# Kernel optimization log

Hardware: AMD Instinct MI355X
Metric: run time of the kernel (lower is better)

## Reference

```python
import jax, jax.numpy as jnp
import numpy as np

NUM, K = 5, 3
IN_DIM, D_OUT = 512, 512
N_U, BATCH, GATED_IN = 64, 8192, 576
NB = NUM + K + 1  # 9 basis channels (num+k splines + 1 SiLU base)
TERM_SIZES = (4, 8)
TERM_MULTS = (32768, 16384)  # 4*32768 + 8*16384 = 262144 = D_OUT*IN_DIM
WDIM = 128


def extend_grid(grid, k):
    # grid: (S, num+1) -> (S, num+1+2k), appending k knots each side with uniform spacing h
    h = (grid[:, -1:] - grid[:, :1]) / (grid.shape[1] - 1)
    left = grid[:, :1] + h * jnp.arange(-k, 0, dtype=grid.dtype)
    right = grid[:, -1:] + h * jnp.arange(1, k + 1, dtype=grid.dtype)
    return jnp.concatenate([left, grid, right], axis=1)


def B_batch(x, grid, k):
    # Cox-de-Boor recursion. x: (S, B), grid: (S, G) extended. Returns (S, G-k-1, B).
    xg = x[:, None, :]
    g = grid[:, :, None]
    v = ((xg >= g[:, :-1]) & (xg < g[:, 1:])).astype(x.dtype)
    for p in range(1, k + 1):
        v = (xg - g[:, :-(p + 1)]) / (g[:, p:-1] - g[:, :-(p + 1)]) * v[:, :-1] \
          + (g[:, p + 1:] - xg) / (g[:, p + 1:] - g[:, 1:-p]) * v[:, 1:]
    return v


def lazy_P(terms, mults, perm, w):
    # emlp-style lazy equivariant projector: permute rows, apply small block
    # projectors with multiplicities, un-permute. w: (R, C).
    invperm = jnp.argsort(perm)
    wp = w[perm]
    outs, off = [], 0
    for P, m in zip(terms, mults):
        s = P.shape[0]
        blk = wp[off:off + m * s].reshape(m, s, -1)
        outs.append(jnp.einsum('ij,mjc->mic', P, blk).reshape(m * s, -1))
        off += m * s
    return jnp.concatenate(outs, axis=0)[invperm]


def setup_inputs() -> dict:
    key = jax.random.key(0)
    ks = jax.random.split(key, 12)
    x = jax.random.normal(ks[0], (BATCH, GATED_IN), dtype=jnp.float32)
    grid = jnp.tile(jnp.linspace(-1.0, 1.0, NUM + 1, dtype=jnp.float32)[None, :], (N_U, 1))
    linear_weight = 0.05 * jax.random.normal(ks[1], (D_OUT, NB * IN_DIM), dtype=jnp.float32)
    linear_bias = 0.05 * jax.random.normal(ks[2], (D_OUT,), dtype=jnp.float32)
    P_term_a = 0.3 * jax.random.normal(ks[3], (TERM_SIZES[0], TERM_SIZES[0]), dtype=jnp.float32)
    P_term_b = 0.3 * jax.random.normal(ks[4], (TERM_SIZES[1], TERM_SIZES[1]), dtype=jnp.float32)
    Pb = (1.0 / np.sqrt(D_OUT)) * jax.random.normal(ks[5], (D_OUT, D_OUT), dtype=jnp.float32)
    bi_basis = 0.01 * jax.random.normal(ks[6], (WDIM, D_OUT, D_OUT), dtype=jnp.float32)
    bi_w = jax.random.normal(ks[7], (WDIM,), dtype=jnp.float32)
    u = jnp.sort(jax.random.randint(ks[8], (N_U,), 0, GATED_IN))
    indices = jax.random.randint(ks[9], (IN_DIM,), 0, N_U)
    perm = jax.random.permutation(ks[10], D_OUT * IN_DIM)
    return {"x": x, "grid": grid, "linear_weight": linear_weight, "linear_bias": linear_bias,
            "P_term_a": P_term_a, "P_term_b": P_term_b, "Pb": Pb,
            "bi_basis": bi_basis, "bi_w": bi_w, "u": u, "indices": indices, "perm": perm}


def reference(x, grid, linear_weight, linear_bias, P_term_a, P_term_b, Pb, bi_basis, bi_w, u, indices, perm):
    batch = x.shape[0]
    # gather gate scalars and build spline + base activations
    gs = x[:, u].T                                   # (S, B)
    eg = extend_grid(grid, K)                        # (S, num+1+2k)
    sp = B_batch(gs, eg, K)                          # (S, num+k, B)
    sp = jnp.transpose(sp, (2, 1, 0))                # (B, num+k, S)
    sb = jax.nn.silu(gs).T[:, None, :]               # (B, 1, S)
    g = jnp.concatenate([sp, sb], axis=1)            # (B, NB, S)
    g = g[:, :, indices]                             # (B, NB, in_dim) gather via inverse indices
    acts = (g * x[:, None, :IN_DIM]).reshape(batch, -1)  # (B, NB*in_dim)
    # equivariant weight projection
    w_r = linear_weight.reshape(D_OUT, NB, IN_DIM).transpose(0, 2, 1).reshape(D_OUT * IN_DIM, NB)
    W_r = lazy_P([P_term_a, P_term_b], TERM_MULTS, perm, w_r)
    W = W_r.reshape(D_OUT, IN_DIM, NB).transpose(0, 2, 1).reshape(D_OUT, NB * IN_DIM)
    b = Pb @ linear_bias
    out = acts @ W.T + b                             # (B, D_OUT)
    # bilinear equivariant mix
    bi_W = jnp.einsum('w,wij->ij', bi_w, bi_basis)   # (D_OUT, D_OUT)
    out = 0.1 * (out @ bi_W.T) + out
    return out
```

## Files before the change

### kernel.cpp

```cpp
#include <hip/hip_runtime.h>

#define DI __device__ __forceinline__

typedef __attribute__((ext_vector_type(8))) short short8;
typedef __attribute__((ext_vector_type(4))) float f32x4;

DI ushort f2bf(float f) {
  union { float f; unsigned u; } v; v.f = f;
  unsigned r = v.u + 0x7fffu + ((v.u >> 16) & 1u);
  return (ushort)(r >> 16);
}

DI void gload_lds16(const void* g, void* l) {
  __builtin_amdgcn_global_load_lds((const __attribute__((address_space(1))) void*)g,
                                   (__attribute__((address_space(3))) void*)l, 16, 0, 0);
}

__global__ __launch_bounds__(256) void k_biW(const float2* __restrict__ bb,
                                             const float* __restrict__ bw,
                                             float2* __restrict__ Mf32,
                                             uint* __restrict__ Mbf16) {
  __shared__ float w[128];
  int tid = threadIdx.x;
  if (tid < 128) w[tid] = bw[tid];
  __syncthreads();
  int t = blockIdx.x * 256 + tid;
  const float2* p = bb + t;
  float ax = 0.f, ay = 0.f;
#pragma unroll 8
  for (int k = 0; k < 128; ++k) {
    float2 v = p[(size_t)k * 131072];
    float s = w[k];
    ax += s * v.x; ay += s * v.y;
  }
  int i = t >> 8, j0 = (t & 255) * 2;
  float2 r;
  r.x = 0.1f * ax + (i == j0 + 0 ? 1.f : 0.f);
  r.y = 0.1f * ay + (i == j0 + 1 ? 1.f : 0.f);
  Mf32[t] = r;
  Mbf16[t] = (uint)f2bf(r.x) | ((uint)f2bf(r.y) << 16);
}

__global__ __launch_bounds__(256) void k_matvec(const float* __restrict__ A,
                                                const float* __restrict__ v,
                                                float* __restrict__ y) {
  int o = blockIdx.x * 4 + (threadIdx.x >> 6);
  int lane = threadIdx.x & 63;
  float acc = 0.f;
  for (int k = lane; k < 512; k += 64) acc += A[o * 512 + k] * v[k];
#pragma unroll
  for (int s = 32; s; s >>= 1) acc += __shfl_down(acc, s, 64);
  if (lane == 0) y[o] = acc;
}

__global__ __launch_bounds__(256) void k_lazyP(const float* __restrict__ LW,
                                               const float* __restrict__ Pa,
                                               const float* __restrict__ Pb8,
                                               const int* __restrict__ perm,
                                               ushort* __restrict__ Wt) {
  int q = blockIdx.x * 256 + threadIdx.x;
  int lane = threadIdx.x & 63;
  int r = perm[q];
  int o = r >> 9, ic = r & 511;
  int a_own = o * 4608 + ic;
  if (q < 131072) {
    int ii = lane & 3, g = lane & ~3;
    float pp[4];
#pragma unroll
    for (int j = 0; j < 4; ++j) pp[j] = Pa[ii * 4 + j];
#pragma unroll
    for (int c = 0; c < 9; ++c) {
      float v = LW[a_own + c * 512];
      float acc = 0.f;
#pragma unroll
      for (int j = 0; j < 4; ++j) acc += pp[j] * __shfl(v, g + j, 64);
      Wt[(size_t)(c * 512 + ic) * 512 + o] = f2bf(acc);
    }
  } else {
    int ii = lane & 7, g = lane & ~7;
    float pp[8];
#pragma unroll
    for (int j = 0; j < 8; ++j) pp[j] = Pb8[ii * 8 + j];
#pragma unroll
    for (int c = 0; c < 9; ++c) {
      float v = LW[a_own + c * 512];
      float acc = 0.f;
#pragma unroll
      for (int j = 0; j < 8; ++j) acc += pp[j] * __shfl(v, g + j, 64);
      Wt[(size_t)(c * 512 + ic) * 512 + o] = f2bf(acc);
    }
  }
}

__global__ __launch_bounds__(256) void k_acts(const float* __restrict__ x,
                                              const float* __restrict__ grid,
                                              const int* __restrict__ u,
                                              const int* __restrict__ indices,
                                              ushort* __restrict__ acts) {
  __shared__ float basis[8][64][9];
  __shared__ int sidx[512];
  int tid = threadIdx.x;
  int b0 = blockIdx.x * 8;
  for (int i = tid; i < 512; i += 256) sidx[i] = indices[i];
#pragma unroll
  for (int e0 = 0; e0 < 2; ++e0) {
    int e = e0 * 256 + tid;
    int row = e >> 6, j = e & 63;
    float gs = x[(size_t)(b0 + row) * 576 + u[j]];
    float g0 = grid[j * 6], g5 = grid[j * 6 + 5];
    float h = (g5 - g0) * 0.2f;
    float lo = g0 - 3.f * h;
    float tt = (gs - lo) / h;
#pragma unroll
    for (int n = 0; n < 8; ++n) basis[row][j][n] = 0.f;
    float fc = floorf(tt);
    int c = (int)fc;
    if (c >= 0 && c <= 10) {
      float t = tt - fc;
      float t2 = t * t, t3 = t2 * t;
      float om = 1.f - t;
      float w0 = t3 * (1.f / 6.f);
      float w1 = (1.f + 3.f * t + 3.f * t2 - 3.f * t3) * (1.f / 6.f);
      float w2 = (4.f - 6.f * t2 + 3.f * t3) * (1.f / 6.f);
      float w3 = om * om * om * (1.f / 6.f);
      if (c <= 7) basis[row][j][c] = w0;
      if (c >= 1 && c <= 8) basis[row][j][c - 1] = w1;
      if (c >= 2 && c <= 9) basis[row][j][c - 2] = w2;
      if (c >= 3) basis[row][j][c - 3] = w3;
    }
    basis[row][j][8] = gs / (1.f + __expf(-gs));
  }
  __syncthreads();
#pragma unroll
  for (int rep = 0; rep < 2; ++rep) {
    int e = rep * 256 + tid;
    int row = e >> 6, i0 = (e & 63) * 8;
    size_t xb = (size_t)(b0 + row) * 576;
    float4 xa = *(const float4*)&x[xb + i0];
    float4 xc = *(const float4*)&x[xb + i0 + 4];
    int4 ja = *(const int4*)&sidx[i0];
    int4 jb = *(const int4*)&sidx[i0 + 4];
    size_t ab = (size_t)(b0 + row) * 4608 + i0;
#pragma unroll
    for (int n = 0; n < 9; ++n) {
      short8 hv;
      hv[0] = (short)f2bf(basis[row][ja.x][n] * xa.x);
      hv[1] = (short)f2bf(basis[row][ja.y][n] * xa.y);
      hv[2] = (short)f2bf(basis[row][ja.z][n] * xa.z);
      hv[3] = (short)f2bf(basis[row][ja.w][n] * xa.w);
      hv[4] = (short)f2bf(basis[row][jb.x][n] * xc.x);
      hv[5] = (short)f2bf(basis[row][jb.y][n] * xc.y);
      hv[6] = (short)f2bf(basis[row][jb.z][n] * xc.z);
      hv[7] = (short)f2bf(basis[row][jb.w][n] * xc.w);
      *(short8*)(&acts[ab + (size_t)n * 512]) = hv;
    }
  }
}

template <int BM, int BN>
__global__ __launch_bounds__(256) void gemm_bt(const ushort* __restrict__ A,
                                               const ushort* __restrict__ B,
                                               ushort* __restrict__ Cout,
                                               int N, int Kd) {
  constexpr int BK = 64;
  constexpr int FM = BM / 32;
  constexpr int FN = BN / 32;
  __shared__ __align__(16) ushort Al[2][BM * BK];
  __shared__ __align__(16) ushort Bl[2][BN * BK];
  int tid = threadIdx.x, lane = tid & 63, wid = tid >> 6;
  int wm = wid >> 1, wn = wid & 1;
  int tiles_n = N / BN;
  int per_xcd = gridDim.x >> 3;
  int flat = (blockIdx.x & 7) * per_xcd + (blockIdx.x >> 3);
  int bm = flat / tiles_n, bn = flat % tiles_n;
  long m0 = (long)bm * BM;
  long n0 = (long)bn * BN;
  int swc = ((tid & 7) ^ ((tid >> 3) & 7)) * 8;
  const ushort* agp = A + (m0 + (tid >> 3)) * (long)Kd + swc;
  const ushort* bgp = B + (n0 + (tid >> 3)) * (long)Kd + swc;

#define STAGE(buf, k0)                                                        \
  do {                                                                        \
    _Pragma("unroll")                                                         \
    for (int it = 0; it < BM / 32; ++it)                                      \
      gload_lds16(agp + (it * 32) * (long)Kd + (k0), &Al[buf][(it * 256 + tid) * 8]); \
    _Pragma("unroll")                                                         \
    for (int it = 0; it < BN / 32; ++it)                                      \
      gload_lds16(bgp + (it * 32) * (long)Kd + (k0), &Bl[buf][(it * 256 + tid) * 8]); \
  } while (0)

  f32x4 acc[FM][FN] = {};
  int swz = (lane & 7) << 3;
  int nt = Kd / BK;
  STAGE(0, 0);
  __syncthreads();
  for (int t = 0; t < nt; ++t) {
    int cur = t & 1;
    if (t + 1 < nt) STAGE(cur ^ 1, (t + 1) * BK);
#pragma unroll
    for (int ks = 0; ks < 2; ++ks) {
      int kidx = (ks * 32 + (lane >> 4) * 8) ^ swz;
      short8 a[FM], b[FN];
#pragma unroll
      for (int f = 0; f < FM; ++f)
        a[f] = *(const short8*)&Al[cur][(wm * (FM * 16) + f * 16 + (lane & 15)) * BK + kidx];
#pragma unroll
      for (int f = 0; f < FN; ++f)
        b[f] = *(const short8*)&Bl[cur][(wn * (FN * 16) + f * 16 + (lane & 15)) * BK + kidx];
#pragma unroll
      for (int i = 0; i < FM; ++i)
#pragma unroll
        for (int j = 0; j < FN; ++j)
          acc[i][j] = __builtin_amdgcn_mfma_f32_16x16x32_bf16(a[i], b[j], acc[i][j], 0, 0, 0);
    }
    __syncthreads();
  }
#undef STAGE
#pragma unroll
  for (int i = 0; i < FM; ++i)
#pragma unroll
    for (int j = 0; j < FN; ++j) {
      int row_b = wm * (FM * 16) + i * 16 + ((lane >> 4) * 4);
      long col = n0 + wn * (FN * 16) + j * 16 + (lane & 15);
#pragma unroll
      for (int r = 0; r < 4; ++r)
        Cout[(m0 + row_b + r) * N + col] = f2bf(acc[i][j][r]);
    }
}

__global__ __launch_bounds__(256, 2) void gemm_sk(const ushort* __restrict__ A,
                                                  const ushort* __restrict__ B,
                                                  float* __restrict__ P0,
                                                  float* __restrict__ P1) {
  constexpr int BM = 128, BN = 128, BK = 64, FM = 4, FN = 4;
  const int Kd = 4608, N = 512;
  __shared__ __align__(16) ushort Al[2][BM * BK];
  __shared__ __align__(16) ushort Bl[2][BN * BK];
  int tid = threadIdx.x, lane = tid & 63, wid = tid >> 6;
  int wm = wid >> 1, wn = wid & 1;
  int per_xcd = gridDim.x >> 3;
  int flat = (blockIdx.x & 7) * per_xcd + (blockIdx.x >> 3);
  int kb = flat >> 8;
  int rem = flat & 255;
  int bm = rem >> 2, bn = rem & 3;
  long m0 = (long)bm * BM;
  long n0 = (long)bn * BN;
  int kbase = kb * (Kd / 2);
  float* Pout = kb ? P1 : P0;

  int swc = ((tid & 7) ^ ((tid >> 3) & 7)) * 8;
  const ushort* agp = A + (m0 + (tid >> 3)) * (long)Kd + kbase + swc;
  const ushort* bgp = B + (n0 + (tid >> 3)) * (long)Kd + kbase + swc;

#define STAGE(buf, k0)                                                        \
  do {                                                                        \
    _Pragma("unroll")                                                         \
    for (int it = 0; it < 4; ++it)                                            \
      gload_lds16(agp + (it * 32) * (long)Kd + (k0), &Al[buf][(it * 256 + tid) * 8]); \
    _Pragma("unroll")                                                         \
    for (int it = 0; it < 4; ++it)                                            \
      gload_lds16(bgp + (it * 32) * (long)Kd + (k0), &Bl[buf][(it * 256 + tid) * 8]); \
  } while (0)

  f32x4 acc[FM][FN] = {};
  int swz = (lane & 7) << 3;
  const int nt = (Kd / 2) / BK;
  STAGE(0, 0);
  __syncthreads();
  for (int t = 0; t < nt; ++t) {
    int cur = t & 1;
    if (t + 1 < nt) STAGE(cur ^ 1, (t + 1) * BK);
#pragma unroll
    for (int ks = 0; ks < 2; ++ks) {
      int kidx = (ks * 32 + (lane >> 4) * 8) ^ swz;
      short8 a[FM], b[FN];
#pragma unroll
      for (int f = 0; f < FM; ++f)
        a[f] = *(const short8*)&Al[cur][(wm * 64 + f * 16 + (lane & 15)) * BK + kidx];
#pragma unroll
      for (int f = 0; f < FN; ++f)
        b[f] = *(const short8*)&Bl[cur][(wn * 64 + f * 16 + (lane & 15)) * BK + kidx];
#pragma unroll
      for (int i = 0; i < FM; ++i)
#pragma unroll
        for (int j = 0; j < FN; ++j)
          acc[i][j] = __builtin_amdgcn_mfma_f32_16x16x32_bf16(a[i], b[j], acc[i][j], 0, 0, 0);
    }
    __syncthreads();
  }
#undef STAGE
#pragma unroll
  for (int i = 0; i < FM; ++i)
#pragma unroll
    for (int j = 0; j < FN; ++j) {
      int row_b = wm * 64 + i * 16 + ((lane >> 4) * 4);
      long col = n0 + wn * 64 + j * 16 + (lane & 15);
#pragma unroll
      for (int r = 0; r < 4; ++r)
        Pout[(m0 + row_b + r) * N + col] = acc[i][j][r];
    }
}

__global__ __launch_bounds__(256) void k_reduce(float4* __restrict__ P0,
                                                const float4* __restrict__ P1,
                                                const float4* __restrict__ b2) {
  int t = blockIdx.x * 256 + threadIdx.x;
#pragma unroll
  for (int rep = 0; rep < 2; ++rep) {
    int e = rep * 524288 + t;
    float4 a = P0[e], b = P1[e], c = b2[e & 127];
    a.x += b.x + c.x; a.y += b.y + c.y; a.z += b.z + c.z; a.w += b.w + c.w;
    P0[e] = a;
  }
}

extern "C" void kernel_launch(void* const* d_in, const int* in_sizes, int n_in,
                              void* d_out, int out_size, void* d_ws, size_t ws_size,
                              hipStream_t stream) {
  const float* x        = (const float*)d_in[0];
  const float* grid     = (const float*)d_in[1];
  const float* LW       = (const float*)d_in[2];
  const float* lb       = (const float*)d_in[3];
  const float* Pa       = (const float*)d_in[4];
  const float* Pb8      = (const float*)d_in[5];
  const float* Pbm      = (const float*)d_in[6];
  const float* bi_basis = (const float*)d_in[7];
  const float* bi_w     = (const float*)d_in[8];
  const int*   u        = (const int*)d_in[9];
  const int*   indices  = (const int*)d_in[10];
  const int*   perm     = (const int*)d_in[11];
  float* out = (float*)d_out;
  char* ws = (char*)d_ws;

  float*  Mf32  = (float*)(ws + 0);
  ushort* Mbf16 = (ushort*)(ws + 1048576);
  float*  tvec  = (float*)(ws + 1572864);
  float*  b2    = (float*)(ws + 1576960);
  ushort* Wt    = (ushort*)(ws + 2097152);
  ushort* W2    = (ushort*)(ws + 6815744);
  ushort* acts  = (ushort*)(ws + 11534336);
  float*  P1    = (float*)(ws + 87031808);

  k_biW<<<512, 256, 0, stream>>>((const float2*)bi_basis, bi_w, (float2*)Mf32, (uint*)Mbf16);
  k_matvec<<<128, 256, 0, stream>>>(Pbm, lb, tvec);
  k_matvec<<<128, 256, 0, stream>>>(Mf32, tvec, b2);
  k_lazyP<<<1024, 256, 0, stream>>>(LW, Pa, Pb8, perm, Wt);
  gemm_bt<128, 128><<<(512 / 128) * (4608 / 128), 256, 0, stream>>>(
      Mbf16, Wt, W2, 4608, 512);
  k_acts<<<1024, 256, 0, stream>>>(x, grid, u, indices, acts);
  gemm_sk<<<512, 256, 0, stream>>>(acts, W2, out, P1);
  k_reduce<<<2048, 256, 0, stream>>>((float4*)out, (const float4*)P1, (const float4*)b2);
}
```

Baseline: 167.2 us.

## Load A fragments directly to registers in split-K GEMM and fold bias

The split-K GEMM no longer stages the A operand (activations) through LDS. Each wave loads its A fragments straight from global memory into registers, double-buffered with the LDS staging of B. Block-to-tile mapping is reordered so the two K halves and four N tiles of one M row sit next to each other for reuse, and the bias add moves from the reduce kernel into the GEMM epilogue of the first K half. This cuts LDS traffic and the footprint per block, but raises register pressure and makes A loads per-lane and less coalesced.

```diff
diff --git a/kernel.cpp b/kernel.cpp
--- a/kernel.cpp
+++ b/kernel.cpp
@@ -15,6 +15,7 @@
   __builtin_amdgcn_global_load_lds((const __attribute__((address_space(1))) void*)g,
                                    (__attribute__((address_space(3))) void*)l, 16, 0, 0);
 }
+
 
 __global__ __launch_bounds__(256) void k_biW(const float2* __restrict__ bb,
                                              const float* __restrict__ bw,
@@ -179,7 +180,7 @@
   const ushort* agp = A + (m0 + (tid >> 3)) * (long)Kd + swc;
   const ushort* bgp = B + (n0 + (tid >> 3)) * (long)Kd + swc;
 
-#define STAGE(buf, k0)                                                        \
+#define STAGE64(buf, k0)                                                      \
   do {                                                                        \
     _Pragma("unroll")                                                         \
     for (int it = 0; it < BM / 32; ++it)                                      \
@@ -192,11 +193,11 @@
   f32x4 acc[FM][FN] = {};
   int swz = (lane & 7) << 3;
   int nt = Kd / BK;
-  STAGE(0, 0);
+  STAGE64(0, 0);
   __syncthreads();
   for (int t = 0; t < nt; ++t) {
     int cur = t & 1;
-    if (t + 1 < nt) STAGE(cur ^ 1, (t + 1) * BK);
+    if (t + 1 < nt) STAGE64(cur ^ 1, (t + 1) * BK);
 #pragma unroll
     for (int ks = 0; ks < 2; ++ks) {
       int kidx = (ks * 32 + (lane >> 4) * 8) ^ swz;
@@ -215,7 +216,7 @@
     }
     __syncthreads();
   }
-#undef STAGE
+#undef STAGE64
 #pragma unroll
   for (int i = 0; i < FM; ++i)
 #pragma unroll
@@ -230,86 +231,96 @@
 
 __global__ __launch_bounds__(256, 2) void gemm_sk(const ushort* __restrict__ A,
                                                   const ushort* __restrict__ B,
+                                                  const float* __restrict__ b2,
                                                   float* __restrict__ P0,
                                                   float* __restrict__ P1) {
-  constexpr int BM = 128, BN = 128, BK = 64, FM = 4, FN = 4;
+  constexpr int BK = 64, FM = 4, FN = 4;
   const int Kd = 4608, N = 512;
-  __shared__ __align__(16) ushort Al[2][BM * BK];
-  __shared__ __align__(16) ushort Bl[2][BN * BK];
+  __shared__ __align__(16) ushort Bl[2][128 * BK];
   int tid = threadIdx.x, lane = tid & 63, wid = tid >> 6;
   int wm = wid >> 1, wn = wid & 1;
-  int per_xcd = gridDim.x >> 3;
-  int flat = (blockIdx.x & 7) * per_xcd + (blockIdx.x >> 3);
-  int kb = flat >> 8;
-  int rem = flat & 255;
-  int bm = rem >> 2, bn = rem & 3;
-  long m0 = (long)bm * BM;
-  long n0 = (long)bn * BN;
-  int kbase = kb * (Kd / 2);
+  int flat = (blockIdx.x & 7) * 64 + (blockIdx.x >> 3);
+  int bm = flat >> 3, kb = (flat >> 2) & 1, bn = flat & 3;
+  long m0 = (long)bm * 128, n0 = (long)bn * 128;
+  int kbase = kb * 2304;
   float* Pout = kb ? P1 : P0;
 
   int swc = ((tid & 7) ^ ((tid >> 3) & 7)) * 8;
-  const ushort* agp = A + (m0 + (tid >> 3)) * (long)Kd + kbase + swc;
   const ushort* bgp = B + (n0 + (tid >> 3)) * (long)Kd + kbase + swc;
-
-#define STAGE(buf, k0)                                                        \
+  const ushort* agp = A + (m0 + wm * 64 + (lane & 15)) * (long)Kd + kbase + (lane >> 4) * 8;
+
+#define STAGEB(buf, k0)                                                       \
   do {                                                                        \
-    _Pragma("unroll")                                                         \
-    for (int it = 0; it < 4; ++it)                                            \
-      gload_lds16(agp + (it * 32) * (long)Kd + (k0), &Al[buf][(it * 256 + tid) * 8]); \
     _Pragma("unroll")                                                         \
     for (int it = 0; it < 4; ++it)                                            \
       gload_lds16(bgp + (it * 32) * (long)Kd + (k0), &Bl[buf][(it * 256 + tid) * 8]); \
   } while (0)
 
+#define LOADA(dst, k0)                                                        \
+  do {                                                                        \
+    _Pragma("unroll")                                                         \
+    for (int ks = 0; ks < 2; ++ks)                                            \
+      _Pragma("unroll")                                                       \
+      for (int f = 0; f < 4; ++f)                                             \
+        dst[ks * 4 + f] = *(const short8*)(agp + (long)f * 16 * Kd + (k0) + ks * 32); \
+  } while (0)
+
+#define COMPUTE(areg, buf)                                                    \
+  do {                                                                        \
+    _Pragma("unroll")                                                         \
+    for (int ks = 0; ks < 2; ++ks) {                                          \
+      int kidx = (ks * 32 + (lane >> 4) * 8) ^ swz;                           \
+      short8 b[FN];                                                           \
+      _Pragma("unroll")                                                       \
+      for (int f = 0; f < FN; ++f)                                            \
+        b[f] = *(const short8*)&Bl[buf][(wn * 64 + f * 16 + (lane & 15)) * BK + kidx]; \
+      _Pragma("unroll")                                                       \
+      for (int i = 0; i < FM; ++i)                                            \
+        _Pragma("unroll")                                                     \
+        for (int j = 0; j < FN; ++j)                                          \
+          acc[i][j] = __builtin_amdgcn_mfma_f32_16x16x32_bf16(areg[ks * 4 + i], b[j], acc[i][j], 0, 0, 0); \
+    }                                                                         \
+  } while (0)
+
   f32x4 acc[FM][FN] = {};
   int swz = (lane & 7) << 3;
-  const int nt = (Kd / 2) / BK;
-  STAGE(0, 0);
+  const int nt = 2304 / BK;
+  short8 aA[8], aB[8];
+  LOADA(aA, 0);
+  STAGEB(0, 0);
   __syncthreads();
-  for (int t = 0; t < nt; ++t) {
-    int cur = t & 1;
-    if (t + 1 < nt) STAGE(cur ^ 1, (t + 1) * BK);
-#pragma unroll
-    for (int ks = 0; ks < 2; ++ks) {
-      int kidx = (ks * 32 + (lane >> 4) * 8) ^ swz;
-      short8 a[FM], b[FN];
-#pragma unroll
-      for (int f = 0; f < FM; ++f)
-        a[f] = *(const short8*)&Al[cur][(wm * 64 + f * 16 + (lane & 15)) * BK + kidx];
-#pragma unroll
-      for (int f = 0; f < FN; ++f)
-        b[f] = *(const short8*)&Bl[cur][(wn * 64 + f * 16 + (lane & 15)) * BK + kidx];
-#pragma unroll
-      for (int i = 0; i < FM; ++i)
-#pragma unroll
-        for (int j = 0; j < FN; ++j)
-          acc[i][j] = __builtin_amdgcn_mfma_f32_16x16x32_bf16(a[i], b[j], acc[i][j], 0, 0, 0);
-    }
+  for (int t = 0; t < nt; t += 2) {
+    if (t + 1 < nt) { LOADA(aB, (t + 1) * BK); STAGEB(1, (t + 1) * BK); }
+    COMPUTE(aA, 0);
     __syncthreads();
-  }
-#undef STAGE
+    if (t + 2 < nt) { LOADA(aA, (t + 2) * BK); STAGEB(0, (t + 2) * BK); }
+    if (t + 1 < nt) COMPUTE(aB, 1);
+    __syncthreads();
+  }
+#undef STAGEB
+#undef LOADA
+#undef COMPUTE
 #pragma unroll
   for (int i = 0; i < FM; ++i)
 #pragma unroll
     for (int j = 0; j < FN; ++j) {
       int row_b = wm * 64 + i * 16 + ((lane >> 4) * 4);
       long col = n0 + wn * 64 + j * 16 + (lane & 15);
+      float bv = (kb == 0) ? b2[col] : 0.f;
 #pragma unroll
       for (int r = 0; r < 4; ++r)
-        Pout[(m0 + row_b + r) * N + col] = acc[i][j][r];
+        Pout[(m0 + row_b + r) * N + col] = acc[i][j][r] + bv;
     }
 }
 
 __global__ __launch_bounds__(256) void k_reduce(float4* __restrict__ P0,
-                                                const float4* __restrict__ P1,
-                                                const float4* __restrict__ b2) {
+                                                const float4* __restrict__ P1) {
   int t = blockIdx.x * 256 + threadIdx.x;
 #pragma unroll
   for (int rep = 0; rep < 2; ++rep) {
     int e = rep * 524288 + t;
-    float4 a = P0[e], b = P1[e], c = b2[e & 127];
-    a.x += b.x + c.x; a.y += b.y + c.y; a.z += b.z + c.z; a.w += b.w + c.w;
+    float4 a = P0[e], b = P1[e];
+    a.x += b.x; a.y += b.y; a.z += b.z; a.w += b.w;
     P0[e] = a;
   }
 }
@@ -348,6 +359,6 @@
   gemm_bt<128, 128><<<(512 / 128) * (4608 / 128), 256, 0, stream>>>(
       Mbf16, Wt, W2, 4608, 512);
   k_acts<<<1024, 256, 0, stream>>>(x, grid, u, indices, acts);
-  gemm_sk<<<512, 256, 0, stream>>>(acts, W2, out, P1);
-  k_reduce<<<2048, 256, 0, stream>>>((float4*)out, (const float4*)P1, (const float4*)b2);
-}
+  gemm_sk<<<512, 256, 0, stream>>>(acts, W2, b2, out, P1);
+  k_reduce<<<2048, 256, 0, stream>>>((float4*)out, (const float4*)P1);
+}
```

Measured after the change: 210.3 us. +25.8%, slower.
